# Kernel tuning notes

Measured on AMD Instinct MI355X. Metric: run time of the kernel, lower is better.

Reference implementation:

```python
import jax, jax.numpy as jnp
import numpy as np

N, C, H, W = 8, 128, 40, 40
EMBED, HEADS = 128, 8
HEAD_DIM = EMBED // HEADS  # 16


def setup_inputs() -> dict:
    key = jax.random.key(0)
    k1, k2, k3 = jax.random.split(key, 3)
    x = jax.random.normal(k1, (N, C, H, W), dtype=jnp.float32)
    # 1x1 conv weights collapsed to matrices
    w_qkv = jax.random.normal(k2, (3 * EMBED, C), dtype=jnp.float32) * (1.0 / np.sqrt(C))
    w_o = jax.random.normal(k3, (C, EMBED), dtype=jnp.float32) * (1.0 / np.sqrt(EMBED))
    b_o = jnp.zeros((C,), dtype=jnp.float32)
    return {"x": x, "w_qkv": w_qkv, "w_o": w_o, "b_o": b_o}


def reference(x, w_qkv, w_o, b_o):
    n, c, h, w = x.shape
    s = h * w  # spatial tokens
    # qkv 1x1 conv: (n, 3*embed, h, w) -> (n, heads, 3, head_dim, s)
    qkv = jnp.einsum('nchw,oc->nohw', x, w_qkv)
    qkv = qkv.reshape(n, HEADS, 3, HEAD_DIM, s)
    q, k, v = qkv[:, :, 0], qkv[:, :, 1], qkv[:, :, 2]  # (n, heads, head_dim, s)
    scale = 1.0 / jnp.sqrt(jnp.asarray(HEAD_DIM, dtype=x.dtype))
    # energy[n,h,i,j] = sum_c q[n,h,c,i] * k[n,h,c,j]
    energy = jnp.einsum('nhci,nhcj->nhij', q, k) * scale
    attn = jax.nn.softmax(energy, axis=-1)  # (n, heads, s, s)
    # out[n,h,c,i] = sum_j attn[n,h,i,j] * v[n,h,c,j]
    out = jnp.einsum('nhij,nhcj->nhci', attn, v)
    out = out.reshape(n, HEADS * HEAD_DIM, h, w)
    o = jnp.einsum('nchw,oc->nohw', out, w_o) + b_o[None, :, None, None]
    return o
```

## Files before the change

kernel.cpp:

```cpp
#include <hip/hip_runtime.h>
#include <hip/hip_bf16.h>

#define NB    8
#define CIN   128
#define SLEN  1600
#define HEADS 8
#define HD    16
#define NH    64
#define VCH   17

#define XT_SUB   (NB * SLEN * CIN)
#define WQ_SUB   (3 * CIN * CIN)
#define WO_SUB   (CIN * CIN)
#define QKV_SUB  (NH * HD * SLEN)
#define VB_SUB   (NH * VCH * SLEN)

#define SCALE_Q 0.36067376022224085f

typedef __attribute__((ext_vector_type(8)))  short  short8;
typedef __attribute__((ext_vector_type(16))) float  f32x16;
typedef __attribute__((ext_vector_type(2)))  unsigned uint2v;

__device__ inline unsigned short f2bf(float f) {
    union { float f; unsigned u; } x; x.f = f;
    unsigned r = x.u + 0x7FFFu + ((x.u >> 16) & 1u);
    return (unsigned short)(r >> 16);
}

__device__ inline unsigned pkbf(float a, float b) {
    __hip_bfloat162 h = __float22bfloat162_rn(make_float2(a, b));
    union { __hip_bfloat162 h; unsigned u; } c; c.h = h; return c.u;
}

__device__ inline short8 mk8(unsigned w0, unsigned w1, unsigned w2, unsigned w3) {
    union { unsigned u[4]; short8 s; } t;
    t.u[0] = w0; t.u[1] = w1; t.u[2] = w2; t.u[3] = w3; return t.s;
}

__global__ __launch_bounds__(64) void cast_kernel(const float* __restrict__ x,
                                                  const float* __restrict__ w_qkv,
                                                  const float* __restrict__ w_o,
                                                  unsigned short* __restrict__ xT,
                                                  unsigned short* __restrict__ wq,
                                                  unsigned short* __restrict__ wo) {
    const int lane = threadIdx.x;
    const int bx = blockIdx.x;
    const int n = blockIdx.y;
    if (bx < 25) {
        const int s = bx * 64 + lane;
        const float* xp = x + n * (CIN * SLEN) + s;
        unsigned short* op = xT + (n * SLEN + s) * CIN;
#pragma unroll 4
        for (int c0 = 0; c0 < CIN; c0 += 8) {
            float v[8];
#pragma unroll
            for (int u = 0; u < 8; ++u) v[u] = xp[(c0 + u) * SLEN];
            union { unsigned short us[8]; uint4 u4; } t;
#pragma unroll
            for (int u = 0; u < 8; ++u) t.us[u] = f2bf(v[u]);
            *(uint4*)(op + c0) = t.u4;
        }
    } else if (n < 2) {
        const float* src = (n == 0) ? w_qkv : w_o;
        unsigned short* dst = (n == 0) ? wq : wo;
        const int cnt = (n == 0) ? WQ_SUB : WO_SUB;
        for (int i = lane * 4; i < cnt; i += 64 * 4) {
            float4 v = *(const float4*)(src + i);
            ushort4 w;
            w.x = f2bf(v.x); w.y = f2bf(v.y); w.z = f2bf(v.z); w.w = f2bf(v.w);
            *(ushort4*)(dst + i) = w;
        }
    }
}

__global__ __launch_bounds__(384) void qkv_gemm(const unsigned short* __restrict__ xT,
                                                const unsigned short* __restrict__ wq,
                                                unsigned short* __restrict__ qT,
                                                unsigned short* __restrict__ kT,
                                                unsigned short* __restrict__ vB) {
    const int tid = threadIdx.x;
    const int wave = tid >> 6;
    const int lane = tid & 63;
    const int l31 = lane & 31, g = lane >> 5;
    const int n = blockIdx.y;
    const int s0 = blockIdx.x * 64;
    const int m0 = wave * 64;

    const unsigned short* Ab = wq + (m0 + l31) * CIN + g * 8;
    const unsigned short* Bb = xT + (n * SLEN + s0 + l31) * CIN + g * 8;

    f32x16 acc00, acc01, acc10, acc11;
#pragma unroll
    for (int e = 0; e < 16; ++e) { acc00[e] = 0.f; acc01[e] = 0.f; acc10[e] = 0.f; acc11[e] = 0.f; }

#pragma unroll
    for (int ks = 0; ks < 8; ++ks) {
        short8 A0 = *(const short8*)(Ab + ks * 16);
        short8 A1 = *(const short8*)(Ab + 32 * CIN + ks * 16);
        short8 B0 = *(const short8*)(Bb + ks * 16);
        short8 B1 = *(const short8*)(Bb + 32 * CIN + ks * 16);
        acc00 = __builtin_amdgcn_mfma_f32_32x32x16_bf16(A0, B0, acc00, 0, 0, 0);
        acc01 = __builtin_amdgcn_mfma_f32_32x32x16_bf16(A0, B1, acc01, 0, 0, 0);
        acc10 = __builtin_amdgcn_mfma_f32_32x32x16_bf16(A1, B0, acc10, 0, 0, 0);
        acc11 = __builtin_amdgcn_mfma_f32_32x32x16_bf16(A1, B1, acc11, 0, 0, 0);
    }

#pragma unroll
    for (int mt = 0; mt < 2; ++mt)
#pragma unroll
        for (int st = 0; st < 2; ++st) {
            f32x16 a = mt ? (st ? acc11 : acc10) : (st ? acc01 : acc00);
            const int s = s0 + st * 32 + l31;
#pragma unroll
            for (int q = 0; q < 4; ++q) {
                int mb = m0 + mt * 32 + 8 * q + 4 * g;
                int h = mb / 48;
                int r48 = mb - h * 48;
                int which = r48 >> 4;
                int c0 = r48 & 15;
                int nh = n * HEADS + h;
                if (which == 2) {
#pragma unroll
                    for (int e = 0; e < 4; ++e)
                        vB[(nh * VCH + c0 + e) * SLEN + s] = f2bf(a[4 * q + e]);
                } else {
                    const float sc = (which == 0) ? SCALE_Q : 1.0f;
                    unsigned short* dst = ((which == 0) ? qT : kT) + nh * (SLEN * HD) + s * HD + c0;
                    ushort4 w;
                    w.x = f2bf(a[4 * q + 0] * sc); w.y = f2bf(a[4 * q + 1] * sc);
                    w.z = f2bf(a[4 * q + 2] * sc); w.w = f2bf(a[4 * q + 3] * sc);
                    *(ushort4*)dst = w;
                }
            }
        }

    if (wave == 0) {
        int s = s0 + lane;
#pragma unroll
        for (int h = 0; h < HEADS; ++h)
            vB[((n * HEADS + h) * VCH + 16) * SLEN + s] = 0x3F80;
    }
}

__global__ __launch_bounds__(128) void out_gemm(const unsigned short* __restrict__ abT,
                                                const unsigned short* __restrict__ wo,
                                                const float* __restrict__ bias,
                                                float* __restrict__ out) {
    const int tid = threadIdx.x;
    const int wave = tid >> 6;
    const int lane = tid & 63;
    const int l31 = lane & 31, g = lane >> 5;
    const int n = blockIdx.y;
    const int s0 = blockIdx.x * 64;
    const int m0 = wave * 64;

    const unsigned short* Ab = wo + (m0 + l31) * CIN + g * 8;
    const unsigned short* Bb = abT + (n * SLEN + s0 + l31) * CIN + g * 8;

    f32x16 acc00, acc01, acc10, acc11;
#pragma unroll
    for (int e = 0; e < 16; ++e) { acc00[e] = 0.f; acc01[e] = 0.f; acc10[e] = 0.f; acc11[e] = 0.f; }

#pragma unroll
    for (int ks = 0; ks < 8; ++ks) {
        short8 A0 = *(const short8*)(Ab + ks * 16);
        short8 A1 = *(const short8*)(Ab + 32 * CIN + ks * 16);
        short8 B0 = *(const short8*)(Bb + ks * 16);
        short8 B1 = *(const short8*)(Bb + 32 * CIN + ks * 16);
        acc00 = __builtin_amdgcn_mfma_f32_32x32x16_bf16(A0, B0, acc00, 0, 0, 0);
        acc01 = __builtin_amdgcn_mfma_f32_32x32x16_bf16(A0, B1, acc01, 0, 0, 0);
        acc10 = __builtin_amdgcn_mfma_f32_32x32x16_bf16(A1, B0, acc10, 0, 0, 0);
        acc11 = __builtin_amdgcn_mfma_f32_32x32x16_bf16(A1, B1, acc11, 0, 0, 0);
    }

#pragma unroll
    for (int mt = 0; mt < 2; ++mt)
#pragma unroll
        for (int st = 0; st < 2; ++st) {
            f32x16 a = mt ? (st ? acc11 : acc10) : (st ? acc01 : acc00);
            const int s = s0 + st * 32 + l31;
#pragma unroll
            for (int q = 0; q < 4; ++q) {
                int mb = m0 + mt * 32 + 8 * q + 4 * g;
                float4 b = *(const float4*)(bias + mb);
                out[(n * CIN + mb + 0) * SLEN + s] = a[4 * q + 0] + b.x;
                out[(n * CIN + mb + 1) * SLEN + s] = a[4 * q + 1] + b.y;
                out[(n * CIN + mb + 2) * SLEN + s] = a[4 * q + 2] + b.z;
                out[(n * CIN + mb + 3) * SLEN + s] = a[4 * q + 3] + b.w;
            }
        }
}

__global__ __launch_bounds__(64) void attn_mfma(const unsigned short* __restrict__ qT,
                                                const unsigned short* __restrict__ kT,
                                                const unsigned short* __restrict__ vB,
                                                unsigned short* __restrict__ abT) {
    const int lane = threadIdx.x;
    const int l31 = lane & 31, g = lane >> 5;
    const int nh = blockIdx.y;
    const int i0 = blockIdx.x * 32;

    const unsigned short* qbase = qT + nh * (SLEN * HD);
    const unsigned short* kptr = kT + nh * (SLEN * HD) + l31 * HD + g * 8;
    const unsigned short* vptr = vB + nh * (VCH * SLEN) + l31 * SLEN + g * 8;

    short8 qf = *(const short8*)(qbase + (i0 + l31) * HD + g * 8);

    f32x16 zz;
#pragma unroll
    for (int e = 0; e < 16; ++e) zz[e] = 0.f;
    f32x16 ov = zz;

    short8 k1 = *(const short8*)kptr;
    short8 vA0 = *(const short8*)vptr;
    short8 vB0 = *(const short8*)(vptr + 16);
    f32x16 sC = __builtin_amdgcn_mfma_f32_32x32x16_bf16(k1, qf, zz, 0, 0, 0);
    k1 = *(const short8*)(kptr + 32 * HD);
    short8 vA1 = *(const short8*)(vptr + 32);
    short8 vB1 = *(const short8*)(vptr + 48);
    const unsigned short* kp2 = kptr + 64 * HD;
    const unsigned short* vp2 = vptr + 64;

    for (int js = 0; js < 50; ++js) {
        short8 k2  = *(const short8*)kp2;
        short8 vA2 = *(const short8*)vp2;
        short8 vB2 = *(const short8*)(vp2 + 16);
        kp2 += 32 * HD; vp2 += 32;

        f32x16 sN = __builtin_amdgcn_mfma_f32_32x32x16_bf16(k1, qf, zz, 0, 0, 0);

        float p[16];
#pragma unroll
        for (int r = 0; r < 16; ++r) p[r] = __builtin_amdgcn_exp2f(sC[r]);

        unsigned P01 = pkbf(p[0], p[1]),   P23 = pkbf(p[2], p[3]);
        unsigned P45 = pkbf(p[4], p[5]),   P67 = pkbf(p[6], p[7]);
        unsigned P89 = pkbf(p[8], p[9]),   P1011 = pkbf(p[10], p[11]);
        unsigned P1213 = pkbf(p[12], p[13]), P1415 = pkbf(p[14], p[15]);

        uint2v s1 = __builtin_amdgcn_permlane32_swap(P01,   P45,   false, false);
        uint2v s2 = __builtin_amdgcn_permlane32_swap(P23,   P67,   false, false);
        uint2v s3 = __builtin_amdgcn_permlane32_swap(P89,   P1213, false, false);
        uint2v s4 = __builtin_amdgcn_permlane32_swap(P1011, P1415, false, false);
        short8 A1 = mk8(s1[0], s2[0], s1[1], s2[1]);
        short8 A2 = mk8(s3[0], s4[0], s3[1], s4[1]);

        ov = __builtin_amdgcn_mfma_f32_32x32x16_bf16(A1, vA0, ov, 0, 0, 0);
        ov = __builtin_amdgcn_mfma_f32_32x32x16_bf16(A2, vB0, ov, 0, 0, 0);

        sC = sN;
        k1 = k2; vA0 = vA1; vB0 = vB1; vA1 = vA2; vB1 = vB2;
    }

    const int src = 16 + (lane & 32);
    const int nb = nh >> 3, h = nh & 7;
#pragma unroll
    for (int e = 0; e < 16; ++e) {
        float r = __shfl(ov[e], src);
        if (l31 < 16) {
            int i = (e & 3) + 8 * (e >> 2) + 4 * g;
            abT[(nb * SLEN + i0 + i) * CIN + h * HD + l31] = f2bf(ov[e] / r);
        }
    }
}

extern "C" void kernel_launch(void* const* d_in, const int* in_sizes, int n_in,
                              void* d_out, int out_size, void* d_ws, size_t ws_size,
                              hipStream_t stream) {
    const float* x     = (const float*)d_in[0];
    const float* w_qkv = (const float*)d_in[1];
    const float* w_o   = (const float*)d_in[2];
    const float* b_o   = (const float*)d_in[3];
    float* out = (float*)d_out;

    unsigned short* xT  = (unsigned short*)d_ws;
    unsigned short* wq  = xT + XT_SUB;
    unsigned short* wo  = wq + WQ_SUB;
    unsigned short* qT  = wo + WO_SUB;
    unsigned short* kT  = qT + QKV_SUB;
    unsigned short* vB  = kT + QKV_SUB;
    unsigned short* abT = vB + VB_SUB;

    cast_kernel<<<dim3(26, NB), 64, 0, stream>>>(x, w_qkv, w_o, xT, wq, wo);
    qkv_gemm<<<dim3(25, NB), 384, 0, stream>>>(xT, wq, qT, kT, vB);
    attn_mfma<<<dim3(50, NH), 64, 0, stream>>>(qT, kT, vB, abT);
    out_gemm<<<dim3(25, NB), 128, 0, stream>>>(abT, wo, b_o, out);
}
```

Baseline: 158.3 us.

## Split attention key range across two waves and shrink GEMM tiles for more blocks

The attention kernel now uses two waves per block, each covering half of the key sequence. Their unnormalized outputs and row sums are combined through shared memory before the final normalization. The cast, QKV and output GEMM kernels get smaller per-wave tiles and more threads or blocks, raising parallelism on a GPU that was under-occupied. This costs some reuse of operand loads per MFMA and adds a shared-memory reduction and a barrier in attention.

```diff
diff --git a/kernel.cpp b/kernel.cpp
--- a/kernel.cpp
+++ b/kernel.cpp
@@ -37,21 +37,22 @@
     t.u[0] = w0; t.u[1] = w1; t.u[2] = w2; t.u[3] = w3; return t.s;
 }
 
-__global__ __launch_bounds__(64) void cast_kernel(const float* __restrict__ x,
-                                                  const float* __restrict__ w_qkv,
-                                                  const float* __restrict__ w_o,
-                                                  unsigned short* __restrict__ xT,
-                                                  unsigned short* __restrict__ wq,
-                                                  unsigned short* __restrict__ wo) {
-    const int lane = threadIdx.x;
+__global__ __launch_bounds__(256) void cast_kernel(const float* __restrict__ x,
+                                                   const float* __restrict__ w_qkv,
+                                                   const float* __restrict__ w_o,
+                                                   unsigned short* __restrict__ xT,
+                                                   unsigned short* __restrict__ wq,
+                                                   unsigned short* __restrict__ wo) {
+    const int tid = threadIdx.x;
     const int bx = blockIdx.x;
     const int n = blockIdx.y;
     if (bx < 25) {
-        const int s = bx * 64 + lane;
+        const int s = bx * 64 + (tid & 63);
+        const int c_base = (tid >> 6) * 32;
         const float* xp = x + n * (CIN * SLEN) + s;
         unsigned short* op = xT + (n * SLEN + s) * CIN;
-#pragma unroll 4
-        for (int c0 = 0; c0 < CIN; c0 += 8) {
+#pragma unroll
+        for (int c0 = c_base; c0 < c_base + 32; c0 += 8) {
             float v[8];
 #pragma unroll
             for (int u = 0; u < 8; ++u) v[u] = xp[(c0 + u) * SLEN];
@@ -64,7 +65,7 @@
         const float* src = (n == 0) ? w_qkv : w_o;
         unsigned short* dst = (n == 0) ? wq : wo;
         const int cnt = (n == 0) ? WQ_SUB : WO_SUB;
-        for (int i = lane * 4; i < cnt; i += 64 * 4) {
+        for (int i = tid * 4; i < cnt; i += 256 * 4) {
             float4 v = *(const float4*)(src + i);
             ushort4 w;
             w.x = f2bf(v.x); w.y = f2bf(v.y); w.z = f2bf(v.z); w.w = f2bf(v.w);
@@ -83,66 +84,61 @@
     const int lane = tid & 63;
     const int l31 = lane & 31, g = lane >> 5;
     const int n = blockIdx.y;
-    const int s0 = blockIdx.x * 64;
+    const int s0 = blockIdx.x * 32;
     const int m0 = wave * 64;
 
     const unsigned short* Ab = wq + (m0 + l31) * CIN + g * 8;
     const unsigned short* Bb = xT + (n * SLEN + s0 + l31) * CIN + g * 8;
 
-    f32x16 acc00, acc01, acc10, acc11;
-#pragma unroll
-    for (int e = 0; e < 16; ++e) { acc00[e] = 0.f; acc01[e] = 0.f; acc10[e] = 0.f; acc11[e] = 0.f; }
+    f32x16 acc0, acc1;
+#pragma unroll
+    for (int e = 0; e < 16; ++e) { acc0[e] = 0.f; acc1[e] = 0.f; }
 
 #pragma unroll
     for (int ks = 0; ks < 8; ++ks) {
         short8 A0 = *(const short8*)(Ab + ks * 16);
         short8 A1 = *(const short8*)(Ab + 32 * CIN + ks * 16);
         short8 B0 = *(const short8*)(Bb + ks * 16);
-        short8 B1 = *(const short8*)(Bb + 32 * CIN + ks * 16);
-        acc00 = __builtin_amdgcn_mfma_f32_32x32x16_bf16(A0, B0, acc00, 0, 0, 0);
-        acc01 = __builtin_amdgcn_mfma_f32_32x32x16_bf16(A0, B1, acc01, 0, 0, 0);
-        acc10 = __builtin_amdgcn_mfma_f32_32x32x16_bf16(A1, B0, acc10, 0, 0, 0);
-        acc11 = __builtin_amdgcn_mfma_f32_32x32x16_bf16(A1, B1, acc11, 0, 0, 0);
-    }
-
-#pragma unroll
-    for (int mt = 0; mt < 2; ++mt)
-#pragma unroll
-        for (int st = 0; st < 2; ++st) {
-            f32x16 a = mt ? (st ? acc11 : acc10) : (st ? acc01 : acc00);
-            const int s = s0 + st * 32 + l31;
-#pragma unroll
-            for (int q = 0; q < 4; ++q) {
-                int mb = m0 + mt * 32 + 8 * q + 4 * g;
-                int h = mb / 48;
-                int r48 = mb - h * 48;
-                int which = r48 >> 4;
-                int c0 = r48 & 15;
-                int nh = n * HEADS + h;
-                if (which == 2) {
-#pragma unroll
-                    for (int e = 0; e < 4; ++e)
-                        vB[(nh * VCH + c0 + e) * SLEN + s] = f2bf(a[4 * q + e]);
-                } else {
-                    const float sc = (which == 0) ? SCALE_Q : 1.0f;
-                    unsigned short* dst = ((which == 0) ? qT : kT) + nh * (SLEN * HD) + s * HD + c0;
-                    ushort4 w;
-                    w.x = f2bf(a[4 * q + 0] * sc); w.y = f2bf(a[4 * q + 1] * sc);
-                    w.z = f2bf(a[4 * q + 2] * sc); w.w = f2bf(a[4 * q + 3] * sc);
-                    *(ushort4*)dst = w;
-                }
+        acc0 = __builtin_amdgcn_mfma_f32_32x32x16_bf16(A0, B0, acc0, 0, 0, 0);
+        acc1 = __builtin_amdgcn_mfma_f32_32x32x16_bf16(A1, B0, acc1, 0, 0, 0);
+    }
+
+    const int s = s0 + l31;
+#pragma unroll
+    for (int mt = 0; mt < 2; ++mt) {
+        f32x16 a = mt ? acc1 : acc0;
+#pragma unroll
+        for (int q = 0; q < 4; ++q) {
+            int mb = m0 + mt * 32 + 8 * q + 4 * g;
+            int h = mb / 48;
+            int r48 = mb - h * 48;
+            int which = r48 >> 4;
+            int c0 = r48 & 15;
+            int nh = n * HEADS + h;
+            if (which == 2) {
+#pragma unroll
+                for (int e = 0; e < 4; ++e)
+                    vB[(nh * VCH + c0 + e) * SLEN + s] = f2bf(a[4 * q + e]);
+            } else {
+                const float sc = (which == 0) ? SCALE_Q : 1.0f;
+                unsigned short* dst = ((which == 0) ? qT : kT) + nh * (SLEN * HD) + s * HD + c0;
+                ushort4 w;
+                w.x = f2bf(a[4 * q + 0] * sc); w.y = f2bf(a[4 * q + 1] * sc);
+                w.z = f2bf(a[4 * q + 2] * sc); w.w = f2bf(a[4 * q + 3] * sc);
+                *(ushort4*)dst = w;
             }
         }
-
-    if (wave == 0) {
-        int s = s0 + lane;
+    }
+
+    if (wave == 0 && lane < 32) {
+        int ss = s0 + lane;
 #pragma unroll
         for (int h = 0; h < HEADS; ++h)
-            vB[((n * HEADS + h) * VCH + 16) * SLEN + s] = 0x3F80;
-    }
-}
-
-__global__ __launch_bounds__(128) void out_gemm(const unsigned short* __restrict__ abT,
+            vB[((n * HEADS + h) * VCH + 16) * SLEN + ss] = 0x3F80;
+    }
+}
+
+__global__ __launch_bounds__(256) void out_gemm(const unsigned short* __restrict__ abT,
                                                 const unsigned short* __restrict__ wo,
                                                 const float* __restrict__ bias,
                                                 float* __restrict__ out) {
@@ -151,58 +147,52 @@
     const int lane = tid & 63;
     const int l31 = lane & 31, g = lane >> 5;
     const int n = blockIdx.y;
-    const int s0 = blockIdx.x * 64;
-    const int m0 = wave * 64;
+    const int s0 = blockIdx.x * 32;
+    const int m0 = wave * 32;
 
     const unsigned short* Ab = wo + (m0 + l31) * CIN + g * 8;
     const unsigned short* Bb = abT + (n * SLEN + s0 + l31) * CIN + g * 8;
 
-    f32x16 acc00, acc01, acc10, acc11;
-#pragma unroll
-    for (int e = 0; e < 16; ++e) { acc00[e] = 0.f; acc01[e] = 0.f; acc10[e] = 0.f; acc11[e] = 0.f; }
+    f32x16 acc;
+#pragma unroll
+    for (int e = 0; e < 16; ++e) acc[e] = 0.f;
 
 #pragma unroll
     for (int ks = 0; ks < 8; ++ks) {
         short8 A0 = *(const short8*)(Ab + ks * 16);
-        short8 A1 = *(const short8*)(Ab + 32 * CIN + ks * 16);
         short8 B0 = *(const short8*)(Bb + ks * 16);
-        short8 B1 = *(const short8*)(Bb + 32 * CIN + ks * 16);
-        acc00 = __builtin_amdgcn_mfma_f32_32x32x16_bf16(A0, B0, acc00, 0, 0, 0);
-        acc01 = __builtin_amdgcn_mfma_f32_32x32x16_bf16(A0, B1, acc01, 0, 0, 0);
-        acc10 = __builtin_amdgcn_mfma_f32_32x32x16_bf16(A1, B0, acc10, 0, 0, 0);
-        acc11 = __builtin_amdgcn_mfma_f32_32x32x16_bf16(A1, B1, acc11, 0, 0, 0);
-    }
-
-#pragma unroll
-    for (int mt = 0; mt < 2; ++mt)
-#pragma unroll
-        for (int st = 0; st < 2; ++st) {
-            f32x16 a = mt ? (st ? acc11 : acc10) : (st ? acc01 : acc00);
-            const int s = s0 + st * 32 + l31;
-#pragma unroll
-            for (int q = 0; q < 4; ++q) {
-                int mb = m0 + mt * 32 + 8 * q + 4 * g;
-                float4 b = *(const float4*)(bias + mb);
-                out[(n * CIN + mb + 0) * SLEN + s] = a[4 * q + 0] + b.x;
-                out[(n * CIN + mb + 1) * SLEN + s] = a[4 * q + 1] + b.y;
-                out[(n * CIN + mb + 2) * SLEN + s] = a[4 * q + 2] + b.z;
-                out[(n * CIN + mb + 3) * SLEN + s] = a[4 * q + 3] + b.w;
-            }
-        }
-}
-
-__global__ __launch_bounds__(64) void attn_mfma(const unsigned short* __restrict__ qT,
-                                                const unsigned short* __restrict__ kT,
-                                                const unsigned short* __restrict__ vB,
-                                                unsigned short* __restrict__ abT) {
-    const int lane = threadIdx.x;
+        acc = __builtin_amdgcn_mfma_f32_32x32x16_bf16(A0, B0, acc, 0, 0, 0);
+    }
+
+    const int s = s0 + l31;
+#pragma unroll
+    for (int q = 0; q < 4; ++q) {
+        int mb = m0 + 8 * q + 4 * g;
+        float4 b = *(const float4*)(bias + mb);
+        out[(n * CIN + mb + 0) * SLEN + s] = acc[4 * q + 0] + b.x;
+        out[(n * CIN + mb + 1) * SLEN + s] = acc[4 * q + 1] + b.y;
+        out[(n * CIN + mb + 2) * SLEN + s] = acc[4 * q + 2] + b.z;
+        out[(n * CIN + mb + 3) * SLEN + s] = acc[4 * q + 3] + b.w;
+    }
+}
+
+__global__ __launch_bounds__(128) void attn_mfma(const unsigned short* __restrict__ qT,
+                                                 const unsigned short* __restrict__ kT,
+                                                 const unsigned short* __restrict__ vB,
+                                                 unsigned short* __restrict__ abT) {
+    __shared__ float plds[64 * 16];
+
+    const int tid = threadIdx.x;
+    const int wave = tid >> 6;
+    const int lane = tid & 63;
     const int l31 = lane & 31, g = lane >> 5;
     const int nh = blockIdx.y;
     const int i0 = blockIdx.x * 32;
+    const int j0 = wave * 800;
 
     const unsigned short* qbase = qT + nh * (SLEN * HD);
-    const unsigned short* kptr = kT + nh * (SLEN * HD) + l31 * HD + g * 8;
-    const unsigned short* vptr = vB + nh * (VCH * SLEN) + l31 * SLEN + g * 8;
+    const unsigned short* kptr = kT + nh * (SLEN * HD) + (j0 + l31) * HD + g * 8;
+    const unsigned short* vptr = vB + nh * (VCH * SLEN) + l31 * SLEN + j0 + g * 8;
 
     short8 qf = *(const short8*)(qbase + (i0 + l31) * HD + g * 8);
 
@@ -221,7 +211,7 @@
     const unsigned short* kp2 = kptr + 64 * HD;
     const unsigned short* vp2 = vptr + 64;
 
-    for (int js = 0; js < 50; ++js) {
+    for (int js = 0; js < 25; ++js) {
         short8 k2  = *(const short8*)kp2;
         short8 vA2 = *(const short8*)vp2;
         short8 vB2 = *(const short8*)(vp2 + 16);
@@ -252,14 +242,32 @@
         k1 = k2; vA0 = vA1; vB0 = vB1; vA1 = vA2; vB1 = vB2;
     }
 
-    const int src = 16 + (lane & 32);
-    const int nb = nh >> 3, h = nh & 7;
-#pragma unroll
-    for (int e = 0; e < 16; ++e) {
-        float r = __shfl(ov[e], src);
-        if (l31 < 16) {
-            int i = (e & 3) + 8 * (e >> 2) + 4 * g;
-            abT[(nb * SLEN + i0 + i) * CIN + h * HD + l31] = f2bf(ov[e] / r);
+    if (wave == 1) {
+#pragma unroll
+        for (int qq = 0; qq < 4; ++qq) {
+            float4 t;
+            t.x = ov[4 * qq + 0]; t.y = ov[4 * qq + 1];
+            t.z = ov[4 * qq + 2]; t.w = ov[4 * qq + 3];
+            *(float4*)&plds[lane * 16 + 4 * qq] = t;
+        }
+    }
+    __syncthreads();
+    if (wave == 0) {
+#pragma unroll
+        for (int qq = 0; qq < 4; ++qq) {
+            float4 t = *(const float4*)&plds[lane * 16 + 4 * qq];
+            ov[4 * qq + 0] += t.x; ov[4 * qq + 1] += t.y;
+            ov[4 * qq + 2] += t.z; ov[4 * qq + 3] += t.w;
+        }
+        const int src = 16 + (lane & 32);
+        const int nb = nh >> 3, h = nh & 7;
+#pragma unroll
+        for (int e = 0; e < 16; ++e) {
+            float r = __shfl(ov[e], src);
+            if (l31 < 16) {
+                int i = (e & 3) + 8 * (e >> 2) + 4 * g;
+                abT[(nb * SLEN + i0 + i) * CIN + h * HD + l31] = f2bf(ov[e] / r);
+            }
         }
     }
 }
@@ -281,8 +289,8 @@
     unsigned short* vB  = kT + QKV_SUB;
     unsigned short* abT = vB + VB_SUB;
 
-    cast_kernel<<<dim3(26, NB), 64, 0, stream>>>(x, w_qkv, w_o, xT, wq, wo);
-    qkv_gemm<<<dim3(25, NB), 384, 0, stream>>>(xT, wq, qT, kT, vB);
-    attn_mfma<<<dim3(50, NH), 64, 0, stream>>>(qT, kT, vB, abT);
-    out_gemm<<<dim3(25, NB), 128, 0, stream>>>(abT, wo, b_o, out);
-}
+    cast_kernel<<<dim3(26, NB), 256, 0, stream>>>(x, w_qkv, w_o, xT, wq, wo);
+    qkv_gemm<<<dim3(50, NB), 384, 0, stream>>>(xT, wq, qT, kT, vB);
+    attn_mfma<<<dim3(50, NH), 128, 0, stream>>>(qT, kT, vB, abT);
+    out_gemm<<<dim3(50, NB), 256, 0, stream>>>(abT, wo, b_o, out);
+}
```

New measurement: 141.3 us. 1.12x faster.
